# Performance work log

Measured on AMD Instinct MI355X. Metric: run time of the kernel, lower is better.

Reference implementation:

```python
import jax, jax.numpy as jnp
import numpy as np

N_USERS = 100000
N_ITEMS = 50000
DIM = 64
HID = 64
E = 3200000
B = 16384


def setup_inputs() -> dict:
    key = jax.random.key(0)
    ks = jax.random.split(key, 16)
    N = N_USERS + N_ITEMS
    return {
        "users": jax.random.randint(ks[0], (B,), 0, N_USERS),
        "items": jax.random.randint(ks[1], (B,), 0, N_ITEMS),
        "edge_index": jax.random.randint(ks[2], (2, E), 0, N),
        "edge_weight": jax.random.uniform(ks[3], (E,), dtype=jnp.float32),
        # learned parameters
        "U": jax.random.normal(ks[4], (N_USERS, DIM), jnp.float32) * 0.1,
        "I": jax.random.normal(ks[5], (N_ITEMS, DIM), jnp.float32) * 0.1,
        "W0": jax.random.normal(ks[6], (DIM, HID), jnp.float32) / np.sqrt(DIM),
        "b0": jnp.zeros((HID,), jnp.float32),
        "g0": jnp.ones((HID,), jnp.float32),
        "be0": jnp.zeros((HID,), jnp.float32),
        "W1": jax.random.normal(ks[7], (HID, HID), jnp.float32) / np.sqrt(HID),
        "b1": jnp.zeros((HID,), jnp.float32),
        "g1": jnp.ones((HID,), jnp.float32),
        "be1": jnp.zeros((HID,), jnp.float32),
        "Wp": jax.random.normal(ks[8], (HID, DIM), jnp.float32) / np.sqrt(HID),
        "bp": jnp.zeros((DIM,), jnp.float32),
        "bu": jnp.zeros((N_USERS,), jnp.float32),
        "bi": jnp.zeros((N_ITEMS,), jnp.float32),
        "mu": jnp.zeros((), jnp.float32),
    }


def _layernorm(h, g, b, eps=1e-5):
    m = jnp.mean(h, axis=-1, keepdims=True)
    v = jnp.mean(jnp.square(h - m), axis=-1, keepdims=True)
    return (h - m) * jax.lax.rsqrt(v + eps) * g + b


def reference(users, items, edge_index, edge_weight, U, I,
              W0, b0, g0, be0, W1, b1, g1, be1, Wp, bp, bu, bi, mu):
    N = U.shape[0] + I.shape[0]
    x = jnp.concatenate([U, I], axis=0)  # [N, DIM]

    # GCN normalization with added self-loops (torch_geometric gcn_norm)
    loop = jnp.arange(N)
    src = jnp.concatenate([edge_index[0], loop])
    dst = jnp.concatenate([edge_index[1], loop])
    ew = jnp.concatenate([edge_weight, jnp.ones((N,), edge_weight.dtype)])
    deg = jax.ops.segment_sum(ew, dst, num_segments=N)
    dinv = jnp.where(deg > 0, jax.lax.rsqrt(deg), 0.0)
    norm = dinv[src] * ew * dinv[dst]  # [E+N]

    def conv(h, W, b):
        hw = h @ W  # [N, HID]
        msgs = norm[:, None] * hw[src]  # gather: [E+N, HID]
        return jax.ops.segment_sum(msgs, dst, num_segments=N) + b

    # layer 0: conv -> layernorm -> relu -> (dropout=identity, eval) -> residual
    h = x
    h_in = h
    h = conv(h, W0, b0)
    h = jax.nn.relu(_layernorm(h, g0, be0)) + h_in
    # layer 1
    h_in = h
    h = conv(h, W1, b1)
    h = jax.nn.relu(_layernorm(h, g1, be1)) + h_in

    h = h @ Wp + bp  # proj_out: [N, DIM]
    h_user = h[:U.shape[0]]
    h_item = h[U.shape[0]:]

    s = jnp.sum(h_user[users] * h_item[items], axis=-1)
    s = s + bu[users] + bi[items] + mu
    return jnp.clip(s, 1.0, 5.0)
```

## Files before the change

### kernel.cpp

```cpp
#include <hip/hip_runtime.h>

#define NU 100000
#define NI 50000
#define NN 150000
#define D  64
#define CAP 47
#define OVF_MAX 4096

#define BINSHIFT 8
#define BINW 256
#define NBINS 586
#define BINCAP 5848
#define STAGE_CAP 11
#define EPT 4
#define SPILL_CAP 262144
#define BIN_BLOCKS 768

typedef unsigned int uint;
typedef unsigned short ushort;
typedef unsigned char uchar;

__device__ __forceinline__ float half_reduce_add(float v) {
    #pragma unroll
    for (int m = 16; m >= 1; m >>= 1) v += __shfl_xor(v, m, 64);
    return v;
}
__device__ __forceinline__ ushort f2bf(float f) {
    union { float f; uint i; } c; c.f = f;
    uint r = c.i + 0x7FFF + ((c.i >> 16) & 1);
    return (ushort)(r >> 16);
}
__device__ __forceinline__ float lane_bcast(float v, int l) {
    return __int_as_float(__builtin_amdgcn_readlane(__float_as_int(v), l));
}
__device__ __forceinline__ uint enc14(float w) {
    uint b = __float_as_uint(w) + 0x00020000u;
    return b & 0xFFFC0000u;
}
__device__ __forceinline__ float dec14(uint r) {
    return __uint_as_float(r & 0xFFFC0000u);
}
__device__ __forceinline__ void spill_one(int d, uint s, float w,
        uint2* __restrict__ spill, int* __restrict__ spillcnt) {
    int si = atomicAdd(spillcnt, 1);
    if (si < SPILL_CAP) spill[si] = make_uint2(s | enc14(w), (uint)d);
}

__global__ __launch_bounds__(256) void k_bin(
        const int* __restrict__ src, const int* __restrict__ dst,
        const float* __restrict__ ew, int* __restrict__ bincur,
        uint2* __restrict__ binbuf, uint2* __restrict__ spill,
        int* __restrict__ spillcnt, uint2* __restrict__ tail,
        uchar* __restrict__ cnt8, int E) {
    __shared__ uint2 stage[NBINS][STAGE_CAP];
    __shared__ int scnt[NBINS];
    int t = threadIdx.x;
    for (int i = t; i < NBINS; i += 256) scnt[i] = 0;
    __syncthreads();
    const int batch = 256 * EPT;
    for (int base = blockIdx.x * batch; base < E; base += BIN_BLOCKS * batch) {
        int dd[EPT]; uint ss[EPT]; float ww[EPT]; int ok[EPT];
        #pragma unroll
        for (int k = 0; k < EPT; ++k) {
            int e = base + k * 256 + t;
            ok[k] = (e < E);
            if (ok[k]) { dd[k] = dst[e]; ss[k] = (uint)src[e]; ww[k] = ew[e]; }
        }
        #pragma unroll
        for (int k = 0; k < EPT; ++k) {
            if (!ok[k]) continue;
            int bin = dd[k] >> BINSHIFT;
            int slot = atomicAdd(&scnt[bin], 1);
            if (slot < STAGE_CAP) {
                stage[bin][slot] = make_uint2(
                    ss[k] | ((uint)(dd[k] & (BINW - 1)) << 18),
                    (uint)__float_as_int(ww[k]));
            } else {
                spill_one(dd[k], ss[k], ww[k], spill, spillcnt);
            }
        }
        __syncthreads();
        for (int bin = t; bin < NBINS; bin += 256) {
            int c = scnt[bin]; if (c > STAGE_CAP) c = STAGE_CAP;
            while (c >= 8) {
                int b0 = atomicAdd(&bincur[bin], 8);
                if (b0 + 8 <= BINCAP) {
                    uint4* o4 = (uint4*)(binbuf + (size_t)bin * BINCAP + b0);
                    uint2* s2 = &stage[bin][c - 8];
                    o4[0] = make_uint4(s2[0].x, s2[0].y, s2[1].x, s2[1].y);
                    o4[1] = make_uint4(s2[2].x, s2[2].y, s2[3].x, s2[3].y);
                    o4[2] = make_uint4(s2[4].x, s2[4].y, s2[5].x, s2[5].y);
                    o4[3] = make_uint4(s2[6].x, s2[6].y, s2[7].x, s2[7].y);
                } else {
                    for (int j = 0; j < 8; ++j) {
                        uint2 r = stage[bin][c - 8 + j];
                        spill_one((bin << BINSHIFT) + (int)(r.x >> 18),
                                  r.x & 0x3FFFFu, __int_as_float((int)r.y),
                                  spill, spillcnt);
                    }
                }
                c -= 8;
            }
            scnt[bin] = c;
        }
        __syncthreads();
    }
    uchar* cb = cnt8 + (size_t)blockIdx.x * NBINS;
    for (int i = t; i < NBINS; i += 256) cb[i] = (uchar)scnt[i];
    uint2* tb = tail + (size_t)blockIdx.x * (NBINS * 8);
    for (int i = t; i < NBINS * 8; i += 256) tb[i] = stage[i >> 3][i & 7];
}

__global__ __launch_bounds__(256) void k_regroup(
        const int* __restrict__ bincur, const uint2* __restrict__ binbuf,
        const uint2* __restrict__ spill, const int* __restrict__ spillcnt,
        const uint2* __restrict__ tail, const uchar* __restrict__ cnt8,
        uint* __restrict__ recs, int* __restrict__ cursor,
        float* __restrict__ dinv, int4* __restrict__ ovf,
        int* __restrict__ ovfcnt) {
    __shared__ uint image[256 * CAP];
    __shared__ int cnt[256];
    __shared__ float ovfw[256];
    int t = threadIdx.x;
    int bin = blockIdx.x;
    cnt[t] = 0; ovfw[t] = 0.0f;
    __syncthreads();
    int dbase = bin << BINSHIFT;
    int nrec = bincur[bin]; if (nrec > BINCAP) nrec = BINCAP;
    const uint2* bb = binbuf + (size_t)bin * BINCAP;
    for (int i = t; i < nrec; i += 256) {
        uint2 r = bb[i];
        int dl = (int)(r.x >> 18);
        int slot = atomicAdd(&cnt[dl], 1);
        uint s = r.x & 0x3FFFFu;
        float w = __int_as_float((int)r.y);
        if (slot < CAP) image[dl * CAP + slot] = enc14(w) | s;
        else {
            atomicAdd(&ovfw[dl], w);
            int o = atomicAdd(ovfcnt, 1);
            if (o < OVF_MAX)
                ovf[o] = make_int4(dbase + dl, (int)s, __float_as_int(w), 0);
        }
    }
    for (int g = t; g < BIN_BLOCKS; g += 256) {
        int c = cnt8[(size_t)g * NBINS + bin];
        const uint2* tb = tail + ((size_t)g * NBINS + bin) * 8;
        for (int j = 0; j < c; ++j) {
            uint2 r = tb[j];
            int dl = (int)(r.x >> 18);
            int slot = atomicAdd(&cnt[dl], 1);
            uint s = r.x & 0x3FFFFu;
            float w = __int_as_float((int)r.y);
            if (slot < CAP) image[dl * CAP + slot] = enc14(w) | s;
            else {
                atomicAdd(&ovfw[dl], w);
                int o = atomicAdd(ovfcnt, 1);
                if (o < OVF_MAX)
                    ovf[o] = make_int4(dbase + dl, (int)s, __float_as_int(w), 0);
            }
        }
    }
    int ns = spillcnt[0]; if (ns > SPILL_CAP) ns = SPILL_CAP;
    for (int i = t; i < ns; i += 256) {
        uint2 e = spill[i];
        int d = (int)e.y;
        if (d < dbase || d >= dbase + BINW) continue;
        int dl = d - dbase;
        int slot = atomicAdd(&cnt[dl], 1);
        if (slot < CAP) image[dl * CAP + slot] = e.x;
        else {
            float w = dec14(e.x);
            atomicAdd(&ovfw[dl], w);
            int o = atomicAdd(ovfcnt, 1);
            if (o < OVF_MAX) ovf[o] = make_int4(d, (int)(e.x & 0x3FFFFu),
                                                __float_as_int(w), 0);
        }
    }
    __syncthreads();
    int ndl = NN - dbase; if (ndl > 256) ndl = 256;
    if (ndl <= 0) return;
    if (t < ndl) {
        int c = cnt[t];
        cursor[dbase + t] = c;
        if (c > CAP) c = CAP;
        float dg = ovfw[t];
        for (int j = 0; j < c; ++j) dg += dec14(image[t * CAP + j]);
        dinv[dbase + t] = rsqrtf(dg + 1.0f);
    }
    int tot = ndl * CAP;
    uint* out = recs + (size_t)dbase * CAP;
    for (int i = t; i < tot; i += 256) out[i] = image[i];
}

__global__ __launch_bounds__(256) void k_gemm1(
        const float* __restrict__ U, const float* __restrict__ I,
        const float* __restrict__ W, const float* __restrict__ dinv,
        ushort* __restrict__ out) {
    int lane = threadIdx.x & 63;
    float wreg[64];
    #pragma unroll
    for (int k = 0; k < 64; ++k) wreg[k] = W[k * 64 + lane];
    int wpb = blockDim.x >> 6;
    int wid = blockIdx.x * wpb + (threadIdx.x >> 6);
    int tw = gridDim.x * wpb;
    for (int n = wid; n < NN; n += tw) {
        float xv = (n < NU) ? U[(size_t)n * D + lane]
                            : I[(size_t)(n - NU) * D + lane];
        float a0 = 0.f, a1 = 0.f, a2 = 0.f, a3 = 0.f;
        #pragma unroll
        for (int k = 0; k < 64; k += 4) {
            a0 = fmaf(lane_bcast(xv, k + 0), wreg[k + 0], a0);
            a1 = fmaf(lane_bcast(xv, k + 1), wreg[k + 1], a1);
            a2 = fmaf(lane_bcast(xv, k + 2), wreg[k + 2], a2);
            a3 = fmaf(lane_bcast(xv, k + 3), wreg[k + 3], a3);
        }
        out[(size_t)n * D + lane] = f2bf(((a0 + a1) + (a2 + a3)) * dinv[n]);
    }
}

__device__ __forceinline__ float2 conv_accum2(int n, int lane,
        const uint* __restrict__ hw2p, const int* __restrict__ cursor,
        const uint* __restrict__ recs, const int4* __restrict__ ovf,
        const int* __restrict__ ovfcnt) {
    int cnt = __builtin_amdgcn_readfirstlane(cursor[n]);
    if (cnt > CAP) cnt = CAP;
    uint rv = (lane < cnt) ? recs[(size_t)n * CAP + lane] : 0u;
    const int  vodd4 = (lane >> 5) << 2;
    const uint lb4   = (uint)(lane & 31) << 2;
    uint xs = *(const uint*)((const char*)hw2p + (((uint)n << 7) + lb4));
    float ax = 0.f, ay = 0.f;
    int cp = (cnt + 7) & ~7;

#define CA_DECL(c) uint x##c##0, x##c##1, x##c##2, x##c##3, \
                        w##c##0, w##c##1, w##c##2, w##c##3;
#define CA_GET(c, i, P) { \
    uint r = (uint)__builtin_amdgcn_ds_bpermute(vodd4 + 8 * (P), (int)rv); \
    w##c##i = r & 0xFFFC0000u; \
    x##c##i = *(const uint*)((const char*)hw2p + \
                             (((r & 0x3FFFFu) << 7) + lb4)); }
#define CA_ISSUE(c, P0) { CA_GET(c, 0, (P0)+0) CA_GET(c, 1, (P0)+1) \
                          CA_GET(c, 2, (P0)+2) CA_GET(c, 3, (P0)+3) }
#define CA_FMA1(c, i) { \
    ax = fmaf(__uint_as_float(w##c##i), __uint_as_float(x##c##i << 16), ax); \
    ay = fmaf(__uint_as_float(w##c##i), \
              __uint_as_float(x##c##i & 0xFFFF0000u), ay); }
#define CA_FMA(c) { CA_FMA1(c,0) CA_FMA1(c,1) CA_FMA1(c,2) CA_FMA1(c,3) }

    CA_DECL(A) CA_DECL(B) CA_DECL(G)
    if (cp > 0)  CA_ISSUE(A, 0)
    if (cp > 8)  CA_ISSUE(B, 4)
    if (cp > 16) CA_ISSUE(G, 8)
    if (cp > 0)  CA_FMA(A)
    if (cp > 24) CA_ISSUE(A, 12)
    if (cp > 8)  CA_FMA(B)
    if (cp > 32) CA_ISSUE(B, 16)
    if (cp > 16) CA_FMA(G)
    if (cp > 40) CA_ISSUE(G, 20)
    if (cp > 24) CA_FMA(A)
    if (cp > 32) CA_FMA(B)
    if (cp > 40) CA_FMA(G)
#undef CA_FMA
#undef CA_FMA1
#undef CA_ISSUE
#undef CA_GET
#undef CA_DECL

    ax += __shfl_xor(ax, 32, 64);
    ay += __shfl_xor(ay, 32, 64);
    ax += __uint_as_float(xs << 16);
    ay += __uint_as_float(xs & 0xFFFF0000u);
    int novf = __builtin_amdgcn_readfirstlane(ovfcnt[0]);
    if (novf > 0) {
        if (novf > OVF_MAX) novf = OVF_MAX;
        for (int j = 0; j < novf; ++j) {
            int4 e = ovf[j];
            if (e.x == n) {
                float w = __int_as_float(e.z);
                uint x = hw2p[(size_t)e.y * 32 + (lane & 31)];
                ax = fmaf(w, __int_as_float((int)(x << 16)), ax);
                ay = fmaf(w, __int_as_float((int)(x & 0xFFFF0000u)), ay);
            }
        }
    }
    return make_float2(ax, ay);
}

__device__ __forceinline__ float2 ln_relu2(float2 a, float di, int p,
        const float* __restrict__ b, const float* __restrict__ g,
        const float* __restrict__ be) {
    float2 bb = ((const float2*)b)[p];
    float v0 = fmaf(a.x, di, bb.x);
    float v1 = fmaf(a.y, di, bb.y);
    float m = half_reduce_add(v0 + v1) * (1.0f / 64.0f);
    float d0 = v0 - m, d1 = v1 - m;
    float var = half_reduce_add(d0 * d0 + d1 * d1) * (1.0f / 64.0f);
    float rs = rsqrtf(var + 1e-5f);
    float2 gg = ((const float2*)g)[p];
    float2 ee = ((const float2*)be)[p];
    return make_float2(fmaxf(fmaf(d0 * rs, gg.x, ee.x), 0.0f),
                       fmaxf(fmaf(d1 * rs, gg.y, ee.y), 0.0f));
}

__global__ __launch_bounds__(256) void k_conv1(
        const uint* __restrict__ hw2p, const int* __restrict__ cursor,
        const uint* __restrict__ recs, const int4* __restrict__ ovf,
        const int* __restrict__ ovfcnt, const float* __restrict__ dinv,
        const float* __restrict__ b, const float* __restrict__ g,
        const float* __restrict__ be, const float* __restrict__ U,
        const float* __restrict__ I, uint* __restrict__ out1) {
    int lane = threadIdx.x & 63;
    int n = __builtin_amdgcn_readfirstlane(blockIdx.x * 4 + (threadIdx.x >> 6));
    if (n >= NN) return;
    float2 a = conv_accum2(n, lane, hw2p, cursor, recs, ovf, ovfcnt);
    int p = lane & 31;
    float2 y = ln_relu2(a, dinv[n], p, b, g, be);
    const float* R = (n < NU) ? (U + (size_t)n * D) : (I + (size_t)(n - NU) * D);
    float2 rr = ((const float2*)R)[p];
    if (lane < 32) {
        out1[(size_t)n * 32 + p] =
            (uint)f2bf(y.x + rr.x) | ((uint)f2bf(y.y + rr.y) << 16);
    }
}

__global__ __launch_bounds__(256) void k_gemm2(
        const ushort* __restrict__ hb, const float* __restrict__ W,
        const float* __restrict__ dinv, ushort* __restrict__ out) {
    int lane = threadIdx.x & 63;
    float wreg[64];
    #pragma unroll
    for (int k = 0; k < 64; ++k) wreg[k] = W[k * 64 + lane];
    int wpb = blockDim.x >> 6;
    int wid = blockIdx.x * wpb + (threadIdx.x >> 6);
    int tw = gridDim.x * wpb;
    for (int n = wid; n < NN; n += tw) {
        float xv = __uint_as_float((uint)hb[(size_t)n * D + lane] << 16);
        float a0 = 0.f, a1 = 0.f, a2 = 0.f, a3 = 0.f;
        #pragma unroll
        for (int k = 0; k < 64; k += 4) {
            a0 = fmaf(lane_bcast(xv, k + 0), wreg[k + 0], a0);
            a1 = fmaf(lane_bcast(xv, k + 1), wreg[k + 1], a1);
            a2 = fmaf(lane_bcast(xv, k + 2), wreg[k + 2], a2);
            a3 = fmaf(lane_bcast(xv, k + 3), wreg[k + 3], a3);
        }
        out[(size_t)n * D + lane] = f2bf(((a0 + a1) + (a2 + a3)) * dinv[n]);
    }
}

__global__ __launch_bounds__(256) void k_conv2score(
        const uint* __restrict__ hw2p, const int* __restrict__ cursor,
        const uint* __restrict__ recs, const int4* __restrict__ ovf,
        const int* __restrict__ ovfcnt, const float* __restrict__ dinv,
        const float* __restrict__ b, const float* __restrict__ g,
        const float* __restrict__ be, const int* __restrict__ users,
        const int* __restrict__ items, const uint* __restrict__ h1b,
        const float* __restrict__ Wp, const float* __restrict__ bp,
        const float* __restrict__ bu, const float* __restrict__ bi,
        const float* __restrict__ mu, float* __restrict__ out, int B) {
    int lane = threadIdx.x & 63;
    float wreg[64];
    #pragma unroll
    for (int k = 0; k < 64; ++k) wreg[k] = Wp[k * 64 + lane];
    float bpl = bp[lane];
    int q = lane & 31;
    int wpb = blockDim.x >> 6;
    int wid = blockIdx.x * wpb + (threadIdx.x >> 6);
    int tw = gridDim.x * wpb;
    for (int p = wid; p < B; p += tw) {
        int un = users[p];
        int in = NU + items[p];
        int nu = __builtin_amdgcn_readfirstlane(un);
        float2 au = conv_accum2(nu, lane, hw2p, cursor, recs, ovf, ovfcnt);
        float2 yu = ln_relu2(au, dinv[nu], q, b, g, be);
        uint xu = h1b[(size_t)nu * 32 + q];
        float2 hu = make_float2(yu.x + __uint_as_float(xu << 16),
                                yu.y + __uint_as_float(xu & 0xFFFF0000u));
        int ni = __builtin_amdgcn_readfirstlane(in);
        float2 ai = conv_accum2(ni, lane, hw2p, cursor, recs, ovf, ovfcnt);
        float2 yi = ln_relu2(ai, dinv[ni], q, b, g, be);
        uint xi = h1b[(size_t)ni * 32 + q];
        float2 hi = make_float2(yi.x + __uint_as_float(xi << 16),
                                yi.y + __uint_as_float(xi & 0xFFFF0000u));
        float pu = bpl, pi = bpl;
        #pragma unroll
        for (int j = 0; j < 32; ++j) {
            pu = fmaf(lane_bcast(hu.x, j), wreg[2 * j], pu);
            pu = fmaf(lane_bcast(hu.y, j), wreg[2 * j + 1], pu);
            pi = fmaf(lane_bcast(hi.x, j), wreg[2 * j], pi);
            pi = fmaf(lane_bcast(hi.y, j), wreg[2 * j + 1], pi);
        }
        float t = pu * pi;
        #pragma unroll
        for (int m = 32; m >= 1; m >>= 1) t += __shfl_xor(t, m, 64);
        if (lane == 0) {
            t += bu[un] + bi[in - NU] + mu[0];
            out[p] = fminf(fmaxf(t, 1.0f), 5.0f);
        }
    }
}

extern "C" void kernel_launch(void* const* d_in, const int* in_sizes, int n_in,
                              void* d_out, int out_size, void* d_ws, size_t ws_size,
                              hipStream_t stream) {
    const int*   users = (const int*)d_in[0];
    const int*   items = (const int*)d_in[1];
    const int*   ei2   = (const int*)d_in[2];
    const float* ew    = (const float*)d_in[3];
    const float* U     = (const float*)d_in[4];
    const float* I     = (const float*)d_in[5];
    const float* W0    = (const float*)d_in[6];
    const float* b0    = (const float*)d_in[7];
    const float* g0    = (const float*)d_in[8];
    const float* be0   = (const float*)d_in[9];
    const float* W1    = (const float*)d_in[10];
    const float* b1    = (const float*)d_in[11];
    const float* g1    = (const float*)d_in[12];
    const float* be1   = (const float*)d_in[13];
    const float* Wp    = (const float*)d_in[14];
    const float* bp    = (const float*)d_in[15];
    const float* bu    = (const float*)d_in[16];
    const float* bi    = (const float*)d_in[17];
    const float* mu    = (const float*)d_in[18];

    int B = in_sizes[0];
    int E = in_sizes[2] / 2;
    const int* srcp = ei2;
    const int* dstp = ei2 + E;

    char* p = (char*)d_ws;
    auto alloc = [&](size_t bytes) -> char* {
        char* r = p;
        p += (bytes + 255) & ~(size_t)255;
        return r;
    };
    int*    cbuf    = (int*)  alloc((size_t)(NBINS + 8) * 4);
    int*    bincur  = cbuf;
    int*    spillcnt= cbuf + NBINS;
    int*    ovfcnt  = cbuf + NBINS + 1;
    int*    cursor  = (int*)  alloc((size_t)NN * 4);
    float*  dinv    = (float*)alloc((size_t)NN * 4);
    int4*   ovf     = (int4*) alloc((size_t)OVF_MAX * 16);
    uint2*  spill   = (uint2*)alloc((size_t)SPILL_CAP * 8);
    uchar*  cnt8    = (uchar*)alloc((size_t)BIN_BLOCKS * NBINS);
    uint2*  binbuf  = (uint2*)alloc((size_t)NBINS * BINCAP * 8);
    uint*   recs    = (uint*) alloc((size_t)NN * CAP * 4);
    ushort* hw2b    = (ushort*)alloc((size_t)NN * D * 2);
    uint*   h1b     = (uint*) alloc((size_t)NN * 32 * 4);
    const uint* hw2p = (const uint*)hw2b;
    uint2*  tail    = (uint2*)hw2b;

    hipMemsetAsync(cbuf, 0, (size_t)(NBINS + 8) * 4, stream);

    int gW = (NN + 3) / 4;

    k_bin<<<BIN_BLOCKS, 256, 0, stream>>>(srcp, dstp, ew, bincur, binbuf,
                                          spill, spillcnt, tail, cnt8, E);
    k_regroup<<<NBINS, 256, 0, stream>>>(bincur, binbuf, spill, spillcnt,
                                         tail, cnt8, recs, cursor, dinv,
                                         ovf, ovfcnt);

    k_gemm1<<<2048, 256, 0, stream>>>(U, I, W0, dinv, hw2b);
    k_conv1<<<gW, 256, 0, stream>>>(hw2p, cursor, recs, ovf, ovfcnt, dinv,
                                    b0, g0, be0, U, I, h1b);
    k_gemm2<<<2048, 256, 0, stream>>>((const ushort*)h1b, W1, dinv, hw2b);
    k_conv2score<<<1024, 256, 0, stream>>>(hw2p, cursor, recs, ovf, ovfcnt, dinv,
                                           b1, g1, be1, users, items, h1b,
                                           Wp, bp, bu, bi, mu,
                                           (float*)d_out, B);
}
```

Before: 431.1 us.

## Interleave user and item gathers in final conv and move Wp to LDS

The final conv+score kernel now gathers neighbour rows for the user and item nodes together in one interleaved routine. This doubles the number of loads in flight per wave. Wp moves from 64 per-lane registers into shared memory to make room for the extra registers this needs, and the grid doubles to 2048 blocks. The first three gather batches are now issued unconditionally, without checking the neighbour count. That relies on rv being zero for lanes past the count, and it spends extra loads on low-degree nodes.

```diff
diff --git a/kernel.cpp b/kernel.cpp
--- a/kernel.cpp
+++ b/kernel.cpp
@@ -218,6 +218,22 @@
     }
 }
 
+#define CA_DECL(c) uint x##c##0, x##c##1, x##c##2, x##c##3, \
+                        w##c##0, w##c##1, w##c##2, w##c##3;
+#define CA_GET(c, i, P, rvv) { \
+    uint r = (uint)__builtin_amdgcn_ds_bpermute(vodd4 + 8 * (P), (int)(rvv)); \
+    w##c##i = r & 0xFFFC0000u; \
+    x##c##i = *(const uint*)((const char*)hw2p + \
+                             (((r & 0x3FFFFu) << 7) + lb4)); }
+#define CA_ISSUE(c, P0, rvv) { CA_GET(c, 0, (P0)+0, rvv) CA_GET(c, 1, (P0)+1, rvv) \
+                               CA_GET(c, 2, (P0)+2, rvv) CA_GET(c, 3, (P0)+3, rvv) }
+#define CA_FMA1(c, i, axv, ayv) { \
+    axv = fmaf(__uint_as_float(w##c##i), __uint_as_float(x##c##i << 16), axv); \
+    ayv = fmaf(__uint_as_float(w##c##i), \
+               __uint_as_float(x##c##i & 0xFFFF0000u), ayv); }
+#define CA_FMA(c, axv, ayv) { CA_FMA1(c,0,axv,ayv) CA_FMA1(c,1,axv,ayv) \
+                              CA_FMA1(c,2,axv,ayv) CA_FMA1(c,3,axv,ayv) }
+
 __device__ __forceinline__ float2 conv_accum2(int n, int lane,
         const uint* __restrict__ hw2p, const int* __restrict__ cursor,
         const uint* __restrict__ recs, const int4* __restrict__ ovf,
@@ -230,41 +246,17 @@
     uint xs = *(const uint*)((const char*)hw2p + (((uint)n << 7) + lb4));
     float ax = 0.f, ay = 0.f;
     int cp = (cnt + 7) & ~7;
-
-#define CA_DECL(c) uint x##c##0, x##c##1, x##c##2, x##c##3, \
-                        w##c##0, w##c##1, w##c##2, w##c##3;
-#define CA_GET(c, i, P) { \
-    uint r = (uint)__builtin_amdgcn_ds_bpermute(vodd4 + 8 * (P), (int)rv); \
-    w##c##i = r & 0xFFFC0000u; \
-    x##c##i = *(const uint*)((const char*)hw2p + \
-                             (((r & 0x3FFFFu) << 7) + lb4)); }
-#define CA_ISSUE(c, P0) { CA_GET(c, 0, (P0)+0) CA_GET(c, 1, (P0)+1) \
-                          CA_GET(c, 2, (P0)+2) CA_GET(c, 3, (P0)+3) }
-#define CA_FMA1(c, i) { \
-    ax = fmaf(__uint_as_float(w##c##i), __uint_as_float(x##c##i << 16), ax); \
-    ay = fmaf(__uint_as_float(w##c##i), \
-              __uint_as_float(x##c##i & 0xFFFF0000u), ay); }
-#define CA_FMA(c) { CA_FMA1(c,0) CA_FMA1(c,1) CA_FMA1(c,2) CA_FMA1(c,3) }
-
     CA_DECL(A) CA_DECL(B) CA_DECL(G)
-    if (cp > 0)  CA_ISSUE(A, 0)
-    if (cp > 8)  CA_ISSUE(B, 4)
-    if (cp > 16) CA_ISSUE(G, 8)
-    if (cp > 0)  CA_FMA(A)
-    if (cp > 24) CA_ISSUE(A, 12)
-    if (cp > 8)  CA_FMA(B)
-    if (cp > 32) CA_ISSUE(B, 16)
-    if (cp > 16) CA_FMA(G)
-    if (cp > 40) CA_ISSUE(G, 20)
-    if (cp > 24) CA_FMA(A)
-    if (cp > 32) CA_FMA(B)
-    if (cp > 40) CA_FMA(G)
-#undef CA_FMA
-#undef CA_FMA1
-#undef CA_ISSUE
-#undef CA_GET
-#undef CA_DECL
-
+    CA_ISSUE(A, 0, rv) CA_ISSUE(B, 4, rv) CA_ISSUE(G, 8, rv)
+    CA_FMA(A, ax, ay)
+    if (cp > 24) CA_ISSUE(A, 12, rv)
+    CA_FMA(B, ax, ay)
+    if (cp > 32) CA_ISSUE(B, 16, rv)
+    CA_FMA(G, ax, ay)
+    if (cp > 40) CA_ISSUE(G, 20, rv)
+    if (cp > 24) CA_FMA(A, ax, ay)
+    if (cp > 32) CA_FMA(B, ax, ay)
+    if (cp > 40) CA_FMA(G, ax, ay)
     ax += __shfl_xor(ax, 32, 64);
     ay += __shfl_xor(ay, 32, 64);
     ax += __uint_as_float(xs << 16);
@@ -283,6 +275,80 @@
         }
     }
     return make_float2(ax, ay);
+}
+
+#define CB_DECL(p, c) uint p##x##c##0, p##x##c##1, p##x##c##2, p##x##c##3, \
+                           p##w##c##0, p##w##c##1, p##w##c##2, p##w##c##3;
+#define CB_GET(p, c, i, P, rvv) { \
+    uint r = (uint)__builtin_amdgcn_ds_bpermute(vodd4 + 8 * (P), (int)(rvv)); \
+    p##w##c##i = r & 0xFFFC0000u; \
+    p##x##c##i = *(const uint*)((const char*)hw2p + \
+                                (((r & 0x3FFFFu) << 7) + lb4)); }
+#define CB_ISSUE(p, c, P0, rvv) { CB_GET(p,c,0,(P0)+0,rvv) CB_GET(p,c,1,(P0)+1,rvv) \
+                                  CB_GET(p,c,2,(P0)+2,rvv) CB_GET(p,c,3,(P0)+3,rvv) }
+#define CB_FMA1(p, c, i, axv, ayv) { \
+    axv = fmaf(__uint_as_float(p##w##c##i), \
+               __uint_as_float(p##x##c##i << 16), axv); \
+    ayv = fmaf(__uint_as_float(p##w##c##i), \
+               __uint_as_float(p##x##c##i & 0xFFFF0000u), ayv); }
+#define CB_FMA(p, c, axv, ayv) { CB_FMA1(p,c,0,axv,ayv) CB_FMA1(p,c,1,axv,ayv) \
+                                 CB_FMA1(p,c,2,axv,ayv) CB_FMA1(p,c,3,axv,ayv) }
+
+__device__ __forceinline__ void conv_accum2_dual(int nu, int ni, int lane,
+        const uint* __restrict__ hw2p, const int* __restrict__ cursor,
+        const uint* __restrict__ recs, const int4* __restrict__ ovf,
+        const int* __restrict__ ovfcnt, float2* outu, float2* outi) {
+    int cu = __builtin_amdgcn_readfirstlane(cursor[nu]); if (cu > CAP) cu = CAP;
+    int ci = __builtin_amdgcn_readfirstlane(cursor[ni]); if (ci > CAP) ci = CAP;
+    uint rvu = (lane < cu) ? recs[(size_t)nu * CAP + lane] : 0u;
+    uint rvi = (lane < ci) ? recs[(size_t)ni * CAP + lane] : 0u;
+    const int  vodd4 = (lane >> 5) << 2;
+    const uint lb4   = (uint)(lane & 31) << 2;
+    uint xsu = *(const uint*)((const char*)hw2p + (((uint)nu << 7) + lb4));
+    uint xsi = *(const uint*)((const char*)hw2p + (((uint)ni << 7) + lb4));
+    float uax = 0.f, uay = 0.f, iax = 0.f, iay = 0.f;
+    int cpu_ = (cu + 7) & ~7, cpi_ = (ci + 7) & ~7;
+    CB_DECL(u, A) CB_DECL(u, B) CB_DECL(u, G)
+    CB_DECL(i, A) CB_DECL(i, B) CB_DECL(i, G)
+    CB_ISSUE(u, A, 0, rvu) CB_ISSUE(i, A, 0, rvi)
+    CB_ISSUE(u, B, 4, rvu) CB_ISSUE(i, B, 4, rvi)
+    CB_ISSUE(u, G, 8, rvu) CB_ISSUE(i, G, 8, rvi)
+    CB_FMA(u, A, uax, uay) CB_FMA(i, A, iax, iay)
+    if (cpu_ > 24) CB_ISSUE(u, A, 12, rvu)
+    if (cpi_ > 24) CB_ISSUE(i, A, 12, rvi)
+    CB_FMA(u, B, uax, uay) CB_FMA(i, B, iax, iay)
+    if (cpu_ > 32) CB_ISSUE(u, B, 16, rvu)
+    if (cpi_ > 32) CB_ISSUE(i, B, 16, rvi)
+    CB_FMA(u, G, uax, uay) CB_FMA(i, G, iax, iay)
+    if (cpu_ > 40) CB_ISSUE(u, G, 20, rvu)
+    if (cpi_ > 40) CB_ISSUE(i, G, 20, rvi)
+    if (cpu_ > 24) CB_FMA(u, A, uax, uay)
+    if (cpi_ > 24) CB_FMA(i, A, iax, iay)
+    if (cpu_ > 32) CB_FMA(u, B, uax, uay)
+    if (cpi_ > 32) CB_FMA(i, B, iax, iay)
+    if (cpu_ > 40) CB_FMA(u, G, uax, uay)
+    if (cpi_ > 40) CB_FMA(i, G, iax, iay)
+    uax += __shfl_xor(uax, 32, 64); uay += __shfl_xor(uay, 32, 64);
+    iax += __shfl_xor(iax, 32, 64); iay += __shfl_xor(iay, 32, 64);
+    uax += __uint_as_float(xsu << 16); uay += __uint_as_float(xsu & 0xFFFF0000u);
+    iax += __uint_as_float(xsi << 16); iay += __uint_as_float(xsi & 0xFFFF0000u);
+    int novf = __builtin_amdgcn_readfirstlane(ovfcnt[0]);
+    if (novf > 0) {
+        if (novf > OVF_MAX) novf = OVF_MAX;
+        for (int j = 0; j < novf; ++j) {
+            int4 e = ovf[j];
+            if (e.x == nu || e.x == ni) {
+                float w = __int_as_float(e.z);
+                uint x = hw2p[(size_t)e.y * 32 + (lane & 31)];
+                float fx = __uint_as_float(x << 16);
+                float fy = __uint_as_float(x & 0xFFFF0000u);
+                if (e.x == nu) { uax = fmaf(w, fx, uax); uay = fmaf(w, fy, uay); }
+                else           { iax = fmaf(w, fx, iax); iay = fmaf(w, fy, iay); }
+            }
+        }
+    }
+    *outu = make_float2(uax, uay);
+    *outi = make_float2(iax, iay);
 }
 
 __device__ __forceinline__ float2 ln_relu2(float2 a, float di, int p,
@@ -356,44 +422,48 @@
         const float* __restrict__ Wp, const float* __restrict__ bp,
         const float* __restrict__ bu, const float* __restrict__ bi,
         const float* __restrict__ mu, float* __restrict__ out, int B) {
-    int lane = threadIdx.x & 63;
-    float wreg[64];
-    #pragma unroll
-    for (int k = 0; k < 64; ++k) wreg[k] = Wp[k * 64 + lane];
+    __shared__ float wlds[64 * 64];
+    int t = threadIdx.x;
+    for (int i = t; i < 64 * 64; i += 256) wlds[i] = Wp[i];
+    __syncthreads();
+    int lane = t & 63;
     float bpl = bp[lane];
     int q = lane & 31;
     int wpb = blockDim.x >> 6;
-    int wid = blockIdx.x * wpb + (threadIdx.x >> 6);
+    int wid = blockIdx.x * wpb + (t >> 6);
     int tw = gridDim.x * wpb;
     for (int p = wid; p < B; p += tw) {
         int un = users[p];
-        int in = NU + items[p];
+        int in_ = NU + items[p];
         int nu = __builtin_amdgcn_readfirstlane(un);
-        float2 au = conv_accum2(nu, lane, hw2p, cursor, recs, ovf, ovfcnt);
+        int ni = __builtin_amdgcn_readfirstlane(in_);
+        float2 au, ai;
+        conv_accum2_dual(nu, ni, lane, hw2p, cursor, recs, ovf, ovfcnt,
+                         &au, &ai);
         float2 yu = ln_relu2(au, dinv[nu], q, b, g, be);
+        float2 yi = ln_relu2(ai, dinv[ni], q, b, g, be);
         uint xu = h1b[(size_t)nu * 32 + q];
+        uint xi = h1b[(size_t)ni * 32 + q];
         float2 hu = make_float2(yu.x + __uint_as_float(xu << 16),
                                 yu.y + __uint_as_float(xu & 0xFFFF0000u));
-        int ni = __builtin_amdgcn_readfirstlane(in);
-        float2 ai = conv_accum2(ni, lane, hw2p, cursor, recs, ovf, ovfcnt);
-        float2 yi = ln_relu2(ai, dinv[ni], q, b, g, be);
-        uint xi = h1b[(size_t)ni * 32 + q];
         float2 hi = make_float2(yi.x + __uint_as_float(xi << 16),
                                 yi.y + __uint_as_float(xi & 0xFFFF0000u));
         float pu = bpl, pi = bpl;
         #pragma unroll
         for (int j = 0; j < 32; ++j) {
-            pu = fmaf(lane_bcast(hu.x, j), wreg[2 * j], pu);
-            pu = fmaf(lane_bcast(hu.y, j), wreg[2 * j + 1], pu);
-            pi = fmaf(lane_bcast(hi.x, j), wreg[2 * j], pi);
-            pi = fmaf(lane_bcast(hi.y, j), wreg[2 * j + 1], pi);
-        }
-        float t = pu * pi;
+            float w0 = wlds[(2 * j) * 64 + lane];
+            float w1 = wlds[(2 * j + 1) * 64 + lane];
+            pu = fmaf(lane_bcast(hu.x, j), w0, pu);
+            pu = fmaf(lane_bcast(hu.y, j), w1, pu);
+            pi = fmaf(lane_bcast(hi.x, j), w0, pi);
+            pi = fmaf(lane_bcast(hi.y, j), w1, pi);
+        }
+        float dot = pu * pi;
         #pragma unroll
-        for (int m = 32; m >= 1; m >>= 1) t += __shfl_xor(t, m, 64);
+        for (int m = 32; m >= 1; m >>= 1) dot += __shfl_xor(dot, m, 64);
         if (lane == 0) {
-            t += bu[un] + bi[in - NU] + mu[0];
-            out[p] = fminf(fmaxf(t, 1.0f), 5.0f);
+            dot += bu[un] + bi[in_ - NU] + mu[0];
+            out[p] = fminf(fmaxf(dot, 1.0f), 5.0f);
         }
     }
 }
@@ -462,7 +532,7 @@
     k_conv1<<<gW, 256, 0, stream>>>(hw2p, cursor, recs, ovf, ovfcnt, dinv,
                                     b0, g0, be0, U, I, h1b);
     k_gemm2<<<2048, 256, 0, stream>>>((const ushort*)h1b, W1, dinv, hw2b);
-    k_conv2score<<<1024, 256, 0, stream>>>(hw2p, cursor, recs, ovf, ovfcnt, dinv,
+    k_conv2score<<<2048, 256, 0, stream>>>(hw2p, cursor, recs, ovf, ovfcnt, dinv,
                                            b1, g1, be1, users, items, h1b,
                                            Wp, bp, bu, bi, mu,
                                            (float*)d_out, B);
```

New measurement: 419.0 us. 2.8% less time.
